# Performance work log

Hardware: AMD Instinct MI355X
Metric: run time of the kernel (lower is better)

Reference implementation:

```python
import jax, jax.numpy as jnp
import numpy as np

G = 16          # spline grid_size
NT = 32         # num_tiles
NS = 2          # num_states
SD = 8          # state_dim
MAXLEN = 2048.0 # max_seq_len
SPREAD = 2.0    # position_spread
LN_EPS = 1e-5


def cubic_bspline(t):
    t = jnp.abs(t)
    r1 = 2.0 / 3.0 - t * t + 0.5 * t ** 3
    r2 = (1.0 / 6.0) * (2.0 - t) ** 3
    return jnp.where(t < 1.0, r1, jnp.where(t < 2.0, r2, jnp.zeros_like(t)))


def ternary(x):
    return jnp.where(x > 0.3, 1.0, jnp.where(x < -0.3, -1.0, 0.0)).astype(x.dtype)


def setup_inputs() -> dict:
    key = jax.random.key(0)
    ks = jax.random.split(key, 14)
    B, T, D = 4, 2048, 1024
    H = D // 4
    x = jax.random.normal(ks[0], (B, T, D), jnp.float32)
    positions = jnp.broadcast_to(jnp.arange(T, dtype=jnp.float32), (B, T))
    states = jax.random.randint(ks[1], (B, T), 0, NS)
    ln_gamma = jnp.ones((D,), jnp.float32)
    ln_beta = jnp.zeros((D,), jnp.float32)
    W1 = jax.random.normal(ks[2], (D, H), jnp.float32) * (1.0 / np.sqrt(D))
    b1 = jnp.zeros((H,), jnp.float32)
    W2 = jax.random.normal(ks[3], (H, 2), jnp.float32) * (1.0 / np.sqrt(H))
    b2 = jnp.zeros((2,), jnp.float32)
    spline_coeffs = jax.random.normal(ks[4], (NT, G, G, 3), jnp.float32) * 0.5
    spline_scales = jnp.ones((NT,), jnp.float32)
    directions = jax.random.normal(ks[5], (NT, D), jnp.float32) * 0.02
    state_signatures = jax.random.normal(ks[6], (NT, SD), jnp.float32) * 0.1
    state_emb = jax.random.normal(ks[7], (NS, SD), jnp.float32)
    state_mod = jnp.ones((NS, NT), jnp.float32)
    output_scale = jnp.ones((1,), jnp.float32) * 0.1
    return dict(x=x, positions=positions, states=states, ln_gamma=ln_gamma,
                ln_beta=ln_beta, W1=W1, b1=b1, W2=W2, b2=b2,
                spline_coeffs=spline_coeffs, spline_scales=spline_scales,
                directions=directions, state_signatures=state_signatures,
                state_emb=state_emb, state_mod=state_mod, output_scale=output_scale)


def reference(x, positions, states, ln_gamma, ln_beta, W1, b1, W2, b2,
              spline_coeffs, spline_scales, directions, state_signatures,
              state_emb, state_mod, output_scale):
    B, T, D = x.shape
    xf = x.reshape(-1, D)                               # [N, D]
    mu = jnp.mean(xf, axis=-1, keepdims=True)
    var = jnp.mean((xf - mu) ** 2, axis=-1, keepdims=True)
    xn = (xf - mu) / jnp.sqrt(var + LN_EPS) * ln_gamma + ln_beta

    # --- three-way routing ---
    sigs = jnp.sign(directions)                         # ternary signatures [NT, D]
    content = xn @ sigs.T                               # [N, NT]
    pos = positions.reshape(-1)
    pn = pos / MAXLEN * NT
    centers = jnp.arange(NT, dtype=xn.dtype)
    spatial = cubic_bspline((pn[:, None] - centers[None, :]) / SPREAD)  # [N, NT]
    st = states.reshape(-1)
    sv = state_emb[st]                                  # [N, SD]
    temporal = jax.nn.sigmoid(sv @ state_signatures.T)  # [N, NT]
    combined = content * spatial * temporal
    probs = jax.nn.softmax(combined * 5.0, axis=-1)
    tile_idx = jnp.argmax(combined, axis=-1)            # [N]
    tile_weights = jnp.take_along_axis(probs, tile_idx[:, None], axis=1)[:, 0]

    # --- compress to 2D spline coordinates ---
    h = jax.nn.gelu(xn @ W1 + b1, approximate=False)
    comp = jnp.tanh(h @ W2 + b2)                        # [N, 2]
    a, b = comp[:, 0], comp[:, 1]

    # --- ternary 2D spline per winning tile (vectorized dispatch) ---
    idx_a = jnp.clip(((a + 1.0) / 2.0 * G).astype(jnp.int32), 0, G - 1)
    idx_b = jnp.clip(((b + 1.0) / 2.0 * G).astype(jnp.int32), 0, G - 1)
    q = spline_coeffs + jax.lax.stop_gradient(ternary(spline_coeffs) - spline_coeffs)
    cell = q[tile_idx, idx_a, idx_b]                    # [N, 3]
    cs = 2.0 / G
    la = (a + 1.0 - idx_a.astype(a.dtype) * cs) / cs
    lb = (b + 1.0 - idx_b.astype(b.dtype) * cs) / cs
    scale = (cell[:, 0] + cell[:, 1] * la + cell[:, 2] * lb) * spline_scales[tile_idx]
    smod = state_mod[st, tile_idx]
    contrib = (scale * smod)[:, None] * directions[tile_idx]  # [N, D]

    out = x + contrib.reshape(B, T, D) * output_scale   # residual, eval (no dropout)
    return out
```

## Files before the change

### kernel.cpp

```cpp
#include <hip/hip_runtime.h>
#include <math.h>

#define NROWS 8192
#define DD    1024
#define HH    256
#define NTT   32
#define NCOLS 288
#define BM    32
#define BK    64
#define NTHR  576
#define NW    9
#define HPS   292

typedef __attribute__((ext_vector_type(8))) __bf16 bf16x8;
typedef __attribute__((ext_vector_type(4))) float f32x4;
typedef __attribute__((ext_vector_type(8))) unsigned short ushort8_t;

static __device__ __forceinline__ unsigned short f2bf(float f) {
    unsigned int u = __float_as_uint(f);
    unsigned int r = (u + 0x7fffu + ((u >> 16) & 1u)) >> 16;
    return (unsigned short)r;
}

static __device__ __forceinline__ float bf2f(unsigned short u) {
    return __uint_as_float(((unsigned int)u) << 16);
}

static __device__ __forceinline__ float sgnf(float x) {
    return x > 0.0f ? 1.0f : (x < 0.0f ? -1.0f : 0.0f);
}

static __device__ __forceinline__ float ternf(float x) {
    return x > 0.3f ? 1.0f : (x < -0.3f ? -1.0f : 0.0f);
}

static __device__ __forceinline__ float bspline(float u) {
    float t = fabsf(u);
    if (t < 1.0f) return 0.66666666666666663f - t * t + 0.5f * t * t * t;
    if (t < 2.0f) { float w = 2.0f - t; return 0.16666666666666666f * w * w * w; }
    return 0.0f;
}

__global__ __launch_bounds__(256) void k_prep(const float* __restrict__ W1,
                                              const float* __restrict__ dirs,
                                              const float* __restrict__ gamma,
                                              const float* __restrict__ beta,
                                              unsigned short* __restrict__ WT,
                                              float* __restrict__ colsumP,
                                              float* __restrict__ bwP) {
    int bid = blockIdx.x;
    int tid = threadIdx.x;
    if (bid < 256) {
        __shared__ float tile[32][33];
        __shared__ float redg[8][32];
        __shared__ float redb[8][32];
        int ktile = bid & 31;
        int ntile = bid >> 5;
        int tx = tid & 31;
        int ty = tid >> 5;
        float sg = 0.f, sb = 0.f;
#pragma unroll
        for (int i = 0; i < 4; ++i) {
            int k = ktile * 32 + ty + i * 8;
            int n = ntile * 32 + tx;
            float w = W1[(size_t)k * HH + n];
            float gk = gamma[k];
            tile[ty + i * 8][tx] = w * gk;
            sg += w * gk;
            sb += w * beta[k];
        }
        redg[ty][tx] = sg;
        redb[ty][tx] = sb;
        __syncthreads();
#pragma unroll
        for (int i = 0; i < 4; ++i) {
            int n = ntile * 32 + ty + i * 8;
            int k = ktile * 32 + tx;
            WT[(size_t)n * DD + k] = f2bf(tile[tx][ty + i * 8]);
        }
        if (ty == 0) {
            float a = 0.f, c = 0.f;
#pragma unroll
            for (int k = 0; k < 8; ++k) { a += redg[k][tx]; c += redb[k][tx]; }
            int j = ntile * 32 + tx;
            colsumP[ktile * NCOLS + j] = a;
            bwP[ktile * NCOLS + j]     = c;
        }
    } else {
        int r = bid - 256;
        float4 v  = ((const float4*)(dirs + (size_t)r * DD))[tid];
        float4 g  = ((const float4*)gamma)[tid];
        float4 be = ((const float4*)beta)[tid];
        float s0 = sgnf(v.x), s1 = sgnf(v.y), s2 = sgnf(v.z), s3 = sgnf(v.w);
        ushort4 o;
        o.x = f2bf(s0 * g.x); o.y = f2bf(s1 * g.y);
        o.z = f2bf(s2 * g.z); o.w = f2bf(s3 * g.w);
        ((ushort4*)(WT + (size_t)(HH + r) * DD))[tid] = o;
        float ps = s0 * g.x + s1 * g.y + s2 * g.z + s3 * g.w;
        float pb = s0 * be.x + s1 * be.y + s2 * be.z + s3 * be.w;
#pragma unroll
        for (int off = 32; off; off >>= 1) {
            ps += __shfl_xor(ps, off);
            pb += __shfl_xor(pb, off);
        }
        __shared__ float red[8];
        int wid = tid >> 6, lane = tid & 63;
        if (lane == 0) { red[wid] = ps; red[wid + 4] = pb; }
        if (tid < 31) {
            colsumP[(tid + 1) * NCOLS + HH + r] = 0.f;
            bwP[(tid + 1) * NCOLS + HH + r]     = 0.f;
        }
        __syncthreads();
        if (tid == 0) {
            colsumP[HH + r] = red[0] + red[1] + red[2] + red[3];
            bwP[HH + r]     = red[4] + red[5] + red[6] + red[7];
        }
    }
}

__global__ __launch_bounds__(NTHR, 1) void k_fused(
    const float* __restrict__ x, const unsigned short* __restrict__ WT,
    const float* __restrict__ colsumP, const float* __restrict__ bwP,
    const float* __restrict__ positions, const int* __restrict__ states,
    const float* __restrict__ b1, const float* __restrict__ W2,
    const float* __restrict__ b2, const float* __restrict__ spc,
    const float* __restrict__ sps, const float* __restrict__ dirs,
    const float* __restrict__ ssig, const float* __restrict__ semb,
    const float* __restrict__ smod, const float* __restrict__ oscale,
    float* __restrict__ out) {
    __shared__ short Xl[BM * DD];
    __shared__ short Bl[2][NCOLS * BK];
    __shared__ float stats[BM][2];
    __shared__ float Csum_l[NCOLS];
    __shared__ float Bw_l[NCOLS];
    float* HPl = (float*)&Bl[0][0];

    int tid  = threadIdx.x;
    int row0 = blockIdx.x * BM;
    int lane = tid & 63;
    int wid  = tid >> 6;
    int wn = wid;
    int l15 = lane & 15, l4 = lane >> 4;

    if (tid < NCOLS) {
        float a = 0.f;
#pragma unroll 8
        for (int k = 0; k < 32; ++k) a += colsumP[k * NCOLS + tid];
        Csum_l[tid] = a;
    } else if (tid < 2 * NCOLS) {
        int j = tid - NCOLS;
        float c = 0.f;
#pragma unroll 8
        for (int k = 0; k < 32; ++k) c += bwP[k * NCOLS + j];
        Bw_l[j] = c;
    }
    __builtin_amdgcn_sched_barrier(0);

    int rA = tid >> 3;
    int g8 = tid & 7;
    const float* xrow = x + (size_t)(row0 + (rA & 31)) * DD + g8 * 8;
    int xbase = (rA & 31) * 2048 + ((g8 * 16) ^ ((rA & 7) << 4));

    float s = 0.f, sq = 0.f;
    float4 x0a, x0b, x1a, x1b;
    f32x4 acc[2][2];
#pragma unroll
    for (int i = 0; i < 2; ++i)
#pragma unroll
        for (int j = 0; j < 2; ++j) acc[i][j] = (f32x4){0.f, 0.f, 0.f, 0.f};

#define STAGE_B(kt, buf)                                                         \
    {                                                                            \
        _Pragma("unroll")                                                        \
        for (int ci = 0; ci < 4; ++ci) {                                         \
            int li = ci * NTHR + tid;                                            \
            int r  = li >> 3;                                                    \
            int g  = li & 7;                                                     \
            const unsigned short* src =                                          \
                WT + (size_t)r * DD + (kt) * 64 + ((g * 8) ^ ((r & 7) << 3));    \
            __builtin_amdgcn_global_load_lds(                                    \
                (const __attribute__((address_space(1))) void*)(const void*)src, \
                (__attribute__((address_space(3))) void*)(void*)(Bl[buf] + li * 8), \
                16, 0, 0);                                                       \
        }                                                                        \
    }

#define WRITE_A(XA, XB, KT)                                                     \
    if (wid < 4) {                                                              \
        s  += (XA.x + XA.y + XA.z + XA.w) + (XB.x + XB.y + XB.z + XB.w);        \
        sq += (XA.x*XA.x + XA.y*XA.y + XA.z*XA.z + XA.w*XA.w)                   \
            + (XB.x*XB.x + XB.y*XB.y + XB.z*XB.z + XB.w*XB.w);                  \
        ushort8_t w;                                                            \
        w[0] = f2bf(XA.x); w[1] = f2bf(XA.y); w[2] = f2bf(XA.z); w[3] = f2bf(XA.w); \
        w[4] = f2bf(XB.x); w[5] = f2bf(XB.y); w[6] = f2bf(XB.z); w[7] = f2bf(XB.w); \
        *(ushort8_t*)((char*)Xl + xbase + (KT) * 128) = w;                      \
    }

#define COMPUTE(KT, CUR)                                                        \
    _Pragma("unroll")                                                           \
    for (int ks = 0; ks < 2; ++ks) {                                            \
        bf16x8 av[2], bv[2];                                                    \
        _Pragma("unroll")                                                       \
        for (int mf = 0; mf < 2; ++mf) {                                        \
            int ra = mf * 16 + l15;                                             \
            int ca = (KT) * 128 + ((ks * 64 + l4 * 16) ^ ((ra & 7) << 4));      \
            av[mf] = *(const bf16x8*)((const char*)Xl + ra * 2048 + ca);        \
        }                                                                       \
        _Pragma("unroll")                                                       \
        for (int nf = 0; nf < 2; ++nf) {                                        \
            int rb = wn * 32 + nf * 16 + l15;                                   \
            int cb = (ks * 64 + l4 * 16) ^ ((rb & 7) << 4);                     \
            bv[nf] = *(const bf16x8*)((const char*)Bl[CUR] + rb * 128 + cb);    \
        }                                                                       \
        _Pragma("unroll")                                                       \
        for (int mf = 0; mf < 2; ++mf)                                          \
            _Pragma("unroll")                                                   \
            for (int nf = 0; nf < 2; ++nf)                                      \
                acc[mf][nf] = __builtin_amdgcn_mfma_f32_16x16x32_bf16(          \
                    av[mf], bv[nf], acc[mf][nf], 0, 0, 0);                      \
    }

#define STEP(kt, XCa, XCb, XIa, XIb, CUR, NXT)                                  \
    {                                                                           \
        if ((kt) <= 14) STAGE_B((kt) + 1, NXT);                                 \
        __builtin_amdgcn_sched_barrier(0);                                      \
        if ((kt) <= 13 && wid < 4) {                                            \
            XIa = ((const float4*)(xrow + ((kt) + 2) * 64))[0];                 \
            XIb = ((const float4*)(xrow + ((kt) + 2) * 64))[1];                 \
        }                                                                       \
        COMPUTE(kt, CUR);                                                       \
        if ((kt) <= 14) WRITE_A(XCa, XCb, (kt) + 1);                            \
        if ((kt) <= 13) {                                                       \
            if (wid < 4) asm volatile("s_waitcnt vmcnt(2) lgkmcnt(0)" ::: "memory"); \
            else         asm volatile("s_waitcnt vmcnt(0)" ::: "memory");       \
        } else if ((kt) == 14) {                                                \
            if (wid < 4) asm volatile("s_waitcnt vmcnt(0) lgkmcnt(0)" ::: "memory"); \
            else         asm volatile("s_waitcnt vmcnt(0)" ::: "memory");       \
        }                                                                       \
        if ((kt) <= 14) {                                                       \
            __builtin_amdgcn_s_barrier();                                       \
            __builtin_amdgcn_sched_barrier(0);                                  \
        }                                                                       \
    }

    STAGE_B(0, 0);
    __builtin_amdgcn_sched_barrier(0);
    if (wid < 4) {
        x0a = ((const float4*)(xrow))[0];
        x0b = ((const float4*)(xrow))[1];
        x1a = ((const float4*)(xrow + 64))[0];
        x1b = ((const float4*)(xrow + 64))[1];
    }
    WRITE_A(x0a, x0b, 0);
    if (wid < 4) asm volatile("s_waitcnt vmcnt(2) lgkmcnt(0)" ::: "memory");
    else         asm volatile("s_waitcnt vmcnt(0)" ::: "memory");
    __builtin_amdgcn_s_barrier();
    __builtin_amdgcn_sched_barrier(0);

    for (int kt = 0; kt < 16; kt += 2) {
        STEP(kt,     x1a, x1b, x0a, x0b, 0, 1);
        STEP(kt + 1, x0a, x0b, x1a, x1b, 1, 0);
    }
    __syncthreads();

    if (wid < 4) {
        s  += __shfl_xor(s, 1);  s  += __shfl_xor(s, 2);  s  += __shfl_xor(s, 4);
        sq += __shfl_xor(sq, 1); sq += __shfl_xor(sq, 2); sq += __shfl_xor(sq, 4);
        if (g8 == 0) {
            float mu  = s * (1.0f / DD);
            float var = sq * (1.0f / DD) - mu * mu;
            stats[rA][0] = mu;
            stats[rA][1] = rsqrtf(var + 1e-5f);
        }
    }
    __syncthreads();

#pragma unroll
    for (int mf = 0; mf < 2; ++mf) {
#pragma unroll
        for (int nf = 0; nf < 2; ++nf) {
            int colg = wn * 32 + nf * 16 + l15;
            float cs = Csum_l[colg];
            float bw = Bw_l[colg];
            int r0 = mf * 16 + l4 * 4;
#pragma unroll
            for (int i = 0; i < 4; ++i) {
                float mu = stats[r0 + i][0], rs = stats[r0 + i][1];
                HPl[(r0 + i) * HPS + colg] = rs * acc[mf][nf][i] - mu * rs * cs + bw;
            }
        }
    }
    __syncthreads();

    float4 b1v = ((const float4*)b1)[lane];
    float w2a[4], w2b[4];
#pragma unroll
    for (int i = 0; i < 4; ++i) {
        int j = lane * 4 + i;
        w2a[i] = W2[2 * j];
        w2b[i] = W2[2 * j + 1];
    }
    float tvs[2] = {0.f, 0.f};
    if (lane < NTT) {
#pragma unroll
        for (int s2 = 0; s2 < 2; ++s2) {
            float d0 = 0.f;
#pragma unroll
            for (int k = 0; k < 8; ++k) d0 += semb[s2 * 8 + k] * ssig[lane * 8 + k];
            tvs[s2] = 1.0f / (1.0f + expf(-d0));
        }
    }
    float osc = oscale[0];
    float bb0 = b2[0], bb1 = b2[1];

    for (int r = wid; r < BM; r += NW) {
        int row = row0 + r;
        float4 hv = *(const float4*)&HPl[r * HPS + lane * 4];
        float hs[4] = {hv.x, hv.y, hv.z, hv.w};
        float bs[4] = {b1v.x, b1v.y, b1v.z, b1v.w};
        float sa = 0.f, sb2 = 0.f;
#pragma unroll
        for (int i = 0; i < 4; ++i) {
            float h = hs[i] + bs[i];
            float g = 0.5f * h * (1.0f + erff(h * 0.70710678118654752f));
            sa  += g * w2a[i];
            sb2 += g * w2b[i];
        }
#pragma unroll
        for (int off = 32; off; off >>= 1) {
            sa  += __shfl_xor(sa, off);
            sb2 += __shfl_xor(sb2, off);
        }
        float av2 = tanhf(sa + bb0);
        float bv2 = tanhf(sb2 + bb1);

        int st = states[row];
        float comb;
        if (lane < NTT) {
            float content = HPl[r * HPS + HH + lane];
            float pn = positions[row] * ((float)NTT / 2048.0f);
            float spv = bspline((pn - (float)lane) * 0.5f);
            comb = content * spv * tvs[st];
        } else {
            comb = -__builtin_inff();
        }
        int bi = lane;
#pragma unroll
        for (int off = 32; off; off >>= 1) {
            float ov = __shfl_xor(comb, off);
            int   oi = __shfl_xor(bi, off);
            if (ov > comb || (ov == comb && oi < bi)) { comb = ov; bi = oi; }
        }
        int ia = (int)((av2 + 1.0f) * 8.0f); ia = ia < 0 ? 0 : (ia > 15 ? 15 : ia);
        int ib = (int)((bv2 + 1.0f) * 8.0f); ib = ib < 0 ? 0 : (ib > 15 ? 15 : ib);
        const float* cc = spc + (((size_t)bi * 16 + ia) * 16 + ib) * 3;
        float c0 = ternf(cc[0]), c1 = ternf(cc[1]), c2 = ternf(cc[2]);
        float la = (av2 + 1.0f - (float)ia * 0.125f) * 8.0f;
        float lb = (bv2 + 1.0f - (float)ib * 0.125f) * 8.0f;
        float scale = (c0 + c1 * la + c2 * lb) * sps[bi];
        float cr = scale * smod[st * NTT + bi] * osc;

        int swzr = (r & 7) << 4;
        const float4* dr = (const float4*)(dirs + (size_t)bi * DD);
        float4* orow = (float4*)(out + (size_t)row * DD);
#pragma unroll
        for (int i = 0; i < 4; ++i) {
            int idx = i * 64 + lane;
            int byteoff = r * 2048 + ((idx * 8) ^ swzr);
            ushort4 xv = *(const ushort4*)((const char*)Xl + byteoff);
            float4 dv = dr[idx];
            float4 o;
            o.x = fmaf(cr, dv.x, bf2f(xv.x));
            o.y = fmaf(cr, dv.y, bf2f(xv.y));
            o.z = fmaf(cr, dv.z, bf2f(xv.z));
            o.w = fmaf(cr, dv.w, bf2f(xv.w));
            orow[idx] = o;
        }
    }
#undef STAGE_B
#undef WRITE_A
#undef COMPUTE
#undef STEP
}

extern "C" void kernel_launch(void* const* d_in, const int* in_sizes, int n_in,
                              void* d_out, int out_size, void* d_ws, size_t ws_size,
                              hipStream_t stream) {
    const float* x     = (const float*)d_in[0];
    const float* pos   = (const float*)d_in[1];
    const int*   st    = (const int*)d_in[2];
    const float* gam   = (const float*)d_in[3];
    const float* bet   = (const float*)d_in[4];
    const float* W1    = (const float*)d_in[5];
    const float* b1    = (const float*)d_in[6];
    const float* W2    = (const float*)d_in[7];
    const float* b2    = (const float*)d_in[8];
    const float* spc   = (const float*)d_in[9];
    const float* sps   = (const float*)d_in[10];
    const float* dirs  = (const float*)d_in[11];
    const float* ssig  = (const float*)d_in[12];
    const float* semb  = (const float*)d_in[13];
    const float* smod  = (const float*)d_in[14];
    const float* oscal = (const float*)d_in[15];
    float* out = (float*)d_out;

    char* ws = (char*)d_ws;
    unsigned short* WT = (unsigned short*)ws;
    float* colsumP = (float*)(ws + 589824);
    float* bwP     = (float*)(ws + 589824 + 36864);

    k_prep<<<288, 256, 0, stream>>>(W1, dirs, gam, bet, WT, colsumP, bwP);
    k_fused<<<NROWS / BM, NTHR, 0, stream>>>(x, WT, colsumP, bwP, pos, st, b1, W2, b2,
                                             spc, sps, dirs, ssig, semb, smod, oscal, out);
}
```

Measured before the change: 41.31 us.

## Replace LDS-staged double-buffered GEMM with upfront X staging and direct B loads

Removes the software-pipelined loop that staged weight tiles into LDS via global_load_lds with double buffering and interleaved x loads. Instead, 8 waves load and convert the whole 32x1024 x tile into LDS up front, computing LayerNorm stats, while the ninth wave reduces the colsum/bw partials. The MFMA loop then reads B fragments directly from global memory (cached) with no per-step barriers. It also drops the occupancy hint of 1 from launch bounds and gives HPl its own LDS buffer. This trades fewer barriers and simpler code for losing load/compute overlap and relying on L2/L1 for the weight reuse across blocks.

```diff
diff --git a/kernel.cpp b/kernel.cpp
--- a/kernel.cpp
+++ b/kernel.cpp
@@ -7,7 +7,6 @@
 #define NTT   32
 #define NCOLS 288
 #define BM    32
-#define BK    64
 #define NTHR  576
 #define NW    9
 #define HPS   292
@@ -118,7 +117,7 @@
     }
 }
 
-__global__ __launch_bounds__(NTHR, 1) void k_fused(
+__global__ __launch_bounds__(NTHR) void k_fused(
     const float* __restrict__ x, const unsigned short* __restrict__ WT,
     const float* __restrict__ colsumP, const float* __restrict__ bwP,
     const float* __restrict__ positions, const int* __restrict__ states,
@@ -129,11 +128,10 @@
     const float* __restrict__ smod, const float* __restrict__ oscale,
     float* __restrict__ out) {
     __shared__ short Xl[BM * DD];
-    __shared__ short Bl[2][NCOLS * BK];
+    __shared__ float HPl[BM * HPS];
     __shared__ float stats[BM][2];
     __shared__ float Csum_l[NCOLS];
     __shared__ float Bw_l[NCOLS];
-    float* HPl = (float*)&Bl[0][0];
 
     int tid  = threadIdx.x;
     int row0 = blockIdx.x * BM;
@@ -142,138 +140,77 @@
     int wn = wid;
     int l15 = lane & 15, l4 = lane >> 4;
 
-    if (tid < NCOLS) {
-        float a = 0.f;
+    if (wid == 8) {
+        for (int j = lane; j < NCOLS; j += 64) {
+            float a = 0.f, c = 0.f;
 #pragma unroll 8
-        for (int k = 0; k < 32; ++k) a += colsumP[k * NCOLS + tid];
-        Csum_l[tid] = a;
-    } else if (tid < 2 * NCOLS) {
-        int j = tid - NCOLS;
-        float c = 0.f;
-#pragma unroll 8
-        for (int k = 0; k < 32; ++k) c += bwP[k * NCOLS + j];
-        Bw_l[j] = c;
-    }
-    __builtin_amdgcn_sched_barrier(0);
-
-    int rA = tid >> 3;
-    int g8 = tid & 7;
-    const float* xrow = x + (size_t)(row0 + (rA & 31)) * DD + g8 * 8;
-    int xbase = (rA & 31) * 2048 + ((g8 * 16) ^ ((rA & 7) << 4));
-
-    float s = 0.f, sq = 0.f;
-    float4 x0a, x0b, x1a, x1b;
-    f32x4 acc[2][2];
-#pragma unroll
-    for (int i = 0; i < 2; ++i)
-#pragma unroll
-        for (int j = 0; j < 2; ++j) acc[i][j] = (f32x4){0.f, 0.f, 0.f, 0.f};
-
-#define STAGE_B(kt, buf)                                                         \
-    {                                                                            \
-        _Pragma("unroll")                                                        \
-        for (int ci = 0; ci < 4; ++ci) {                                         \
-            int li = ci * NTHR + tid;                                            \
-            int r  = li >> 3;                                                    \
-            int g  = li & 7;                                                     \
-            const unsigned short* src =                                          \
-                WT + (size_t)r * DD + (kt) * 64 + ((g * 8) ^ ((r & 7) << 3));    \
-            __builtin_amdgcn_global_load_lds(                                    \
-                (const __attribute__((address_space(1))) void*)(const void*)src, \
-                (__attribute__((address_space(3))) void*)(void*)(Bl[buf] + li * 8), \
-                16, 0, 0);                                                       \
-        }                                                                        \
-    }
-
-#define WRITE_A(XA, XB, KT)                                                     \
-    if (wid < 4) {                                                              \
-        s  += (XA.x + XA.y + XA.z + XA.w) + (XB.x + XB.y + XB.z + XB.w);        \
-        sq += (XA.x*XA.x + XA.y*XA.y + XA.z*XA.z + XA.w*XA.w)                   \
-            + (XB.x*XB.x + XB.y*XB.y + XB.z*XB.z + XB.w*XB.w);                  \
-        ushort8_t w;                                                            \
-        w[0] = f2bf(XA.x); w[1] = f2bf(XA.y); w[2] = f2bf(XA.z); w[3] = f2bf(XA.w); \
-        w[4] = f2bf(XB.x); w[5] = f2bf(XB.y); w[6] = f2bf(XB.z); w[7] = f2bf(XB.w); \
-        *(ushort8_t*)((char*)Xl + xbase + (KT) * 128) = w;                      \
-    }
-
-#define COMPUTE(KT, CUR)                                                        \
-    _Pragma("unroll")                                                           \
-    for (int ks = 0; ks < 2; ++ks) {                                            \
-        bf16x8 av[2], bv[2];                                                    \
-        _Pragma("unroll")                                                       \
-        for (int mf = 0; mf < 2; ++mf) {                                        \
-            int ra = mf * 16 + l15;                                             \
-            int ca = (KT) * 128 + ((ks * 64 + l4 * 16) ^ ((ra & 7) << 4));      \
-            av[mf] = *(const bf16x8*)((const char*)Xl + ra * 2048 + ca);        \
-        }                                                                       \
-        _Pragma("unroll")                                                       \
-        for (int nf = 0; nf < 2; ++nf) {                                        \
-            int rb = wn * 32 + nf * 16 + l15;                                   \
-            int cb = (ks * 64 + l4 * 16) ^ ((rb & 7) << 4);                     \
-            bv[nf] = *(const bf16x8*)((const char*)Bl[CUR] + rb * 128 + cb);    \
-        }                                                                       \
-        _Pragma("unroll")                                                       \
-        for (int mf = 0; mf < 2; ++mf)                                          \
-            _Pragma("unroll")                                                   \
-            for (int nf = 0; nf < 2; ++nf)                                      \
-                acc[mf][nf] = __builtin_amdgcn_mfma_f32_16x16x32_bf16(          \
-                    av[mf], bv[nf], acc[mf][nf], 0, 0, 0);                      \
-    }
-
-#define STEP(kt, XCa, XCb, XIa, XIb, CUR, NXT)                                  \
-    {                                                                           \
-        if ((kt) <= 14) STAGE_B((kt) + 1, NXT);                                 \
-        __builtin_amdgcn_sched_barrier(0);                                      \
-        if ((kt) <= 13 && wid < 4) {                                            \
-            XIa = ((const float4*)(xrow + ((kt) + 2) * 64))[0];                 \
-            XIb = ((const float4*)(xrow + ((kt) + 2) * 64))[1];                 \
-        }                                                                       \
-        COMPUTE(kt, CUR);                                                       \
-        if ((kt) <= 14) WRITE_A(XCa, XCb, (kt) + 1);                            \
-        if ((kt) <= 13) {                                                       \
-            if (wid < 4) asm volatile("s_waitcnt vmcnt(2) lgkmcnt(0)" ::: "memory"); \
-            else         asm volatile("s_waitcnt vmcnt(0)" ::: "memory");       \
-        } else if ((kt) == 14) {                                                \
-            if (wid < 4) asm volatile("s_waitcnt vmcnt(0) lgkmcnt(0)" ::: "memory"); \
-            else         asm volatile("s_waitcnt vmcnt(0)" ::: "memory");       \
-        }                                                                       \
-        if ((kt) <= 14) {                                                       \
-            __builtin_amdgcn_s_barrier();                                       \
-            __builtin_amdgcn_sched_barrier(0);                                  \
-        }                                                                       \
-    }
-
-    STAGE_B(0, 0);
-    __builtin_amdgcn_sched_barrier(0);
-    if (wid < 4) {
-        x0a = ((const float4*)(xrow))[0];
-        x0b = ((const float4*)(xrow))[1];
-        x1a = ((const float4*)(xrow + 64))[0];
-        x1b = ((const float4*)(xrow + 64))[1];
-    }
-    WRITE_A(x0a, x0b, 0);
-    if (wid < 4) asm volatile("s_waitcnt vmcnt(2) lgkmcnt(0)" ::: "memory");
-    else         asm volatile("s_waitcnt vmcnt(0)" ::: "memory");
-    __builtin_amdgcn_s_barrier();
-    __builtin_amdgcn_sched_barrier(0);
-
-    for (int kt = 0; kt < 16; kt += 2) {
-        STEP(kt,     x1a, x1b, x0a, x0b, 0, 1);
-        STEP(kt + 1, x0a, x0b, x1a, x1b, 1, 0);
-    }
-    __syncthreads();
-
-    if (wid < 4) {
-        s  += __shfl_xor(s, 1);  s  += __shfl_xor(s, 2);  s  += __shfl_xor(s, 4);
-        sq += __shfl_xor(sq, 1); sq += __shfl_xor(sq, 2); sq += __shfl_xor(sq, 4);
-        if (g8 == 0) {
+            for (int k = 0; k < 32; ++k) {
+                a += colsumP[k * NCOLS + j];
+                c += bwP[k * NCOLS + j];
+            }
+            Csum_l[j] = a;
+            Bw_l[j]   = c;
+        }
+    } else {
+        int sr = tid >> 4;
+        int sc = tid & 15;
+        const float4* xsrc = (const float4*)(x + (size_t)(row0 + sr) * DD + sc * 64);
+        int swz = (sr & 7) << 4;
+        char* xdst = (char*)Xl + sr * 2048;
+        float s = 0.f, sq = 0.f;
+#pragma unroll
+        for (int q = 0; q < 8; ++q) {
+            float4 v0 = xsrc[q * 2];
+            float4 v1 = xsrc[q * 2 + 1];
+            s  += (v0.x + v0.y + v0.z + v0.w) + (v1.x + v1.y + v1.z + v1.w);
+            sq += (v0.x*v0.x + v0.y*v0.y + v0.z*v0.z + v0.w*v0.w)
+                + (v1.x*v1.x + v1.y*v1.y + v1.z*v1.z + v1.w*v1.w);
+            ushort8_t w;
+            w[0] = f2bf(v0.x); w[1] = f2bf(v0.y); w[2] = f2bf(v0.z); w[3] = f2bf(v0.w);
+            w[4] = f2bf(v1.x); w[5] = f2bf(v1.y); w[6] = f2bf(v1.z); w[7] = f2bf(v1.w);
+            *(ushort8_t*)(xdst + ((sc * 128 + q * 16) ^ swz)) = w;
+        }
+        s  += __shfl_xor(s, 1);  s  += __shfl_xor(s, 2);
+        s  += __shfl_xor(s, 4);  s  += __shfl_xor(s, 8);
+        sq += __shfl_xor(sq, 1); sq += __shfl_xor(sq, 2);
+        sq += __shfl_xor(sq, 4); sq += __shfl_xor(sq, 8);
+        if (sc == 0) {
             float mu  = s * (1.0f / DD);
             float var = sq * (1.0f / DD) - mu * mu;
-            stats[rA][0] = mu;
-            stats[rA][1] = rsqrtf(var + 1e-5f);
+            stats[sr][0] = mu;
+            stats[sr][1] = rsqrtf(var + 1e-5f);
         }
     }
     __syncthreads();
+
+    const unsigned short* bp0 = WT + (size_t)(wn * 32 + l15) * DD + l4 * 8;
+    const unsigned short* bp1 = bp0 + (size_t)16 * DD;
+    int raby0 = l15 * 2048;
+    int raby1 = (16 + l15) * 2048;
+    int sw = (l15 & 7) << 4;
+
+    f32x4 acc[2][2];
+#pragma unroll
+    for (int i = 0; i < 2; ++i)
+#pragma unroll
+        for (int j = 0; j < 2; ++j) acc[i][j] = (f32x4){0.f, 0.f, 0.f, 0.f};
+
+#pragma unroll 8
+    for (int kt = 0; kt < 16; ++kt) {
+#pragma unroll
+        for (int ks = 0; ks < 2; ++ks) {
+            int cbyte = kt * 128 + ((ks * 64 + l4 * 16) ^ sw);
+            bf16x8 a0 = *(const bf16x8*)((const char*)Xl + raby0 + cbyte);
+            bf16x8 a1 = *(const bf16x8*)((const char*)Xl + raby1 + cbyte);
+            int eoff = kt * 64 + ks * 32;
+            bf16x8 b0 = *(const bf16x8*)(bp0 + eoff);
+            bf16x8 b1 = *(const bf16x8*)(bp1 + eoff);
+            acc[0][0] = __builtin_amdgcn_mfma_f32_16x16x32_bf16(a0, b0, acc[0][0], 0, 0, 0);
+            acc[0][1] = __builtin_amdgcn_mfma_f32_16x16x32_bf16(a0, b1, acc[0][1], 0, 0, 0);
+            acc[1][0] = __builtin_amdgcn_mfma_f32_16x16x32_bf16(a1, b0, acc[1][0], 0, 0, 0);
+            acc[1][1] = __builtin_amdgcn_mfma_f32_16x16x32_bf16(a1, b1, acc[1][1], 0, 0, 0);
+        }
+    }
 
 #pragma unroll
     for (int mf = 0; mf < 2; ++mf) {
@@ -377,10 +314,6 @@
             orow[idx] = o;
         }
     }
-#undef STAGE_B
-#undef WRITE_A
-#undef COMPUTE
-#undef STEP
 }
 
 extern "C" void kernel_launch(void* const* d_in, const int* in_sizes, int n_in,
```

Measured after the change: 51.29 us. 24.2% more time.
